# Optimization experiments

Measured on AMD Instinct MI355X. Metric: run time of the kernel, lower is better.

The kernel has to match this reference:

```python
import jax, jax.numpy as jnp
import numpy as np

B, T, HID, H = 2, 2048, 2048, 16
D = HID // H  # 128


def apply_rope(x):
    # Faithful port of the torch helper: treats x dims as (B, T, H, D)
    # regardless of the caller's actual layout (this reproduces the
    # original module's quirk of rotating q along the head axis).
    b, t, h, d = x.shape
    half = d // 2
    x1, x2 = x[..., :half], x[..., half:]
    theta = 1.0 / (10000.0 ** (jnp.arange(0, half, 2, dtype=jnp.float32) / half))
    pos = jnp.arange(t, dtype=jnp.float32)
    freq = pos[:, None] * theta[None, :]            # (t, half//2)
    sin = jnp.sin(freq)[None, :, None, :]
    cos = jnp.cos(freq)[None, :, None, :]
    x1e, x1o = x1[..., ::2], x1[..., 1::2]
    x2e, x2o = x2[..., ::2], x2[..., 1::2]
    x1r = jnp.concatenate([x1e * cos - x1o * sin, x1e * sin + x1o * cos], axis=-1)
    x2r = jnp.concatenate([x2e * cos - x2o * sin, x2e * sin + x2o * cos], axis=-1)
    return jnp.concatenate([x1r, x2r], axis=-1)


def setup_inputs() -> dict:
    key = jax.random.key(0)
    ks = jax.random.split(key, 5)
    s = 0.02
    return {
        "hidden_states": jax.random.normal(ks[0], (B, T, HID), dtype=jnp.float32),
        "Wq": jax.random.normal(ks[1], (HID, HID), dtype=jnp.float32) * s,
        "Wk": jax.random.normal(ks[2], (D, HID), dtype=jnp.float32) * s,
        "Wv": jax.random.normal(ks[3], (D, HID), dtype=jnp.float32) * s,
        "Wo": jax.random.normal(ks[4], (HID, HID), dtype=jnp.float32) * s,
    }


def reference(hidden_states, Wq, Wk, Wv, Wo):
    b, t, _ = hidden_states.shape
    scaling = D ** -0.5
    # projections (nn.Linear: x @ W.T)
    q = (hidden_states @ Wq.T).reshape(b, t, H, D).transpose(0, 2, 1, 3)  # (B,H,T,D)
    k = hidden_states @ Wk.T                                             # (B,T,D)
    v = hidden_states @ Wv.T                                             # (B,T,D)
    # RoPE applied exactly as in the torch module (note layout quirk)
    q = apply_rope(q)                 # rotated along head axis, as original
    k = apply_rope(k[:, None])        # (B,1,T,D): pos=0 -> permutation only
    v = v[:, None]                    # (B,1,T,D)
    scores = jnp.einsum("bhqd,bokd->bhqk", q, k) * scaling  # (B,H,T,T)
    causal = jnp.tril(jnp.ones((t, t), dtype=bool))
    scores = jnp.where(causal[None, None], scores, -jnp.inf)
    probs = jax.nn.softmax(scores, axis=-1)
    attn = jnp.einsum("bhqk,bokd->bhqd", probs, v)           # (B,H,T,D)
    attn = attn.transpose(0, 2, 1, 3).reshape(b, t, HID)
    return attn @ Wo.T
```

## Files before the change

kernel.cpp:

```cpp
#include <hip/hip_runtime.h>
#include <math.h>


typedef unsigned short u16;
typedef __attribute__((ext_vector_type(8))) short s16x8;
typedef __attribute__((ext_vector_type(4))) float f32x4;

#define B_   2
#define T_   2048
#define HID_ 2048
#define H_   16
#define D_   128

__device__ __forceinline__ u16 f2bf(float f) {
  unsigned u = __float_as_uint(f);
  unsigned r = ((u >> 16) & 1u) + 0x7fffu;
  return (u16)((u + r) >> 16);
}
__device__ __forceinline__ float bf2f(u16 b) {
  return __uint_as_float(((unsigned)b) << 16);
}

__global__ void cast_f32_to_bf16(const float* __restrict__ in,
                                 u16* __restrict__ out, int n4) {
  int i = blockIdx.x * blockDim.x + threadIdx.x;
  if (i >= n4) return;
  float4 v = reinterpret_cast<const float4*>(in)[i];
  ushort4 o;
  o.x = f2bf(v.x); o.y = f2bf(v.y); o.z = f2bf(v.z); o.w = f2bf(v.w);
  reinterpret_cast<ushort4*>(out)[i] = o;
}

__device__ __forceinline__ void gload_lds16(const u16* g, u16* lds) {
  __builtin_amdgcn_global_load_lds(
      (const __attribute__((address_space(1))) void*)g,
      (__attribute__((address_space(3))) void*)lds, 16, 0, 0);
}

template <int OUT_BF16>
__global__ __launch_bounds__(256) void gemm_bt(
    const u16* __restrict__ A, const u16* __restrict__ Bm,
    void* __restrict__ Cv, int M, int N, int K) {
  __shared__ __align__(16) u16 As[128 * 64];
  __shared__ __align__(16) u16 Bs[128 * 64];
  const int tid = threadIdx.x;
  const int w = tid >> 6, l = tid & 63;
  const int bm = blockIdx.x, bn = blockIdx.y;
  const int wm = (w >> 1) * 64, wn = (w & 1) * 64;
  const int lg = l >> 4, lc = l & 15;
  const int srow = l >> 3, slot = l & 7;
  f32x4 acc[4][4] = {};

  for (int k0 = 0; k0 < K; k0 += 64) {
#pragma unroll
    for (int i = 0; i < 4; ++i) {
      int R = (w * 4 + i) * 8;
      int row = R + srow;
      int c = slot ^ (row & 7);
      gload_lds16(A + (size_t)(bm * 128 + row) * K + k0 + c * 8, &As[R * 64]);
      gload_lds16(Bm + (size_t)(bn * 128 + row) * K + k0 + c * 8, &Bs[R * 64]);
    }
    __syncthreads();
#pragma unroll
    for (int kc = 0; kc < 2; ++kc) {
      s16x8 af[4], bfv[4];
#pragma unroll
      for (int mi = 0; mi < 4; ++mi) {
        int r = wm + mi * 16 + lc;
        int cc = kc * 4 + lg;
        af[mi] = *(const s16x8*)((const char*)As + r * 128 + ((cc ^ (r & 7)) * 16));
      }
#pragma unroll
      for (int ni = 0; ni < 4; ++ni) {
        int r = wn + ni * 16 + lc;
        int cc = kc * 4 + lg;
        bfv[ni] = *(const s16x8*)((const char*)Bs + r * 128 + ((cc ^ (r & 7)) * 16));
      }
#pragma unroll
      for (int mi = 0; mi < 4; ++mi)
#pragma unroll
        for (int ni = 0; ni < 4; ++ni)
          acc[mi][ni] = __builtin_amdgcn_mfma_f32_16x16x32_bf16(
              af[mi], bfv[ni], acc[mi][ni], 0, 0, 0);
    }
    __syncthreads();
  }
#pragma unroll
  for (int mi = 0; mi < 4; ++mi)
#pragma unroll
    for (int ni = 0; ni < 4; ++ni) {
      int mrow = bm * 128 + wm + mi * 16 + lg * 4;
      int ncol = bn * 128 + wn + ni * 16 + lc;
#pragma unroll
      for (int r = 0; r < 4; ++r) {
        float v = acc[mi][ni][r];
        if (OUT_BF16)
          ((u16*)Cv)[(size_t)(mrow + r) * N + ncol] = f2bf(v);
        else
          ((float*)Cv)[(size_t)(mrow + r) * N + ncol] = v;
      }
    }
}

__global__ void rope_q(u16* __restrict__ Q) {
  int idx = blockIdx.x * blockDim.x + threadIdx.x;
  int row = idx >> 10;
  int p = idx & 1023;
  int h = p >> 6;
  int i = p & 63;
  int j = i & 31;
  int d = (i < 32) ? (2 * i) : (64 + 2 * (i - 32));
  float theta = exp2f(-(float)j * (13.287712379549449f / 32.0f));
  float ang = (float)h * theta;
  float s, c;
  __sincosf(ang, &s, &c);
  unsigned* pq = (unsigned*)(Q + (size_t)row * HID_ + h * D_ + d);
  unsigned v = *pq;
  float a = bf2f((u16)(v & 0xffffu));
  float b = bf2f((u16)(v >> 16));
  *pq = ((unsigned)f2bf(a * s + b * c) << 16) | (unsigned)f2bf(a * c - b * s);
}

__global__ void transpose_v(const u16* __restrict__ V, u16* __restrict__ Vt) {
  int idx = blockIdx.x * blockDim.x + threadIdx.x;
  int t = idx & (T_ - 1);
  int d = (idx >> 11) & (D_ - 1);
  int b = idx >> 18;
  Vt[idx] = V[(size_t)(b * T_ + t) * D_ + d];
}

__global__ __launch_bounds__(256, 2) void mqa_attn(
    const u16* __restrict__ Q, const u16* __restrict__ K,
    const u16* __restrict__ Vt, u16* __restrict__ O) {
  __shared__ __align__(16) u16 Plds[4][2][16][72];
  const int tid = threadIdx.x;
  const int w = tid >> 6, l = tid & 63;
  const int lg = l >> 4, lc = l & 15;
  const int idx = blockIdx.x * 4 + w;
  const int h = blockIdx.y, b = blockIdx.z;
  const int ga = idx, gb = 127 - idx;
  const int q0a = ga * 16, q0b = gb * 16;
  const int nka = ga / 4 + 1, nkb = gb / 4 + 1;
  const u16* Kp = K + (size_t)b * T_ * D_;
  const u16* Vb = Vt + (size_t)b * D_ * T_;

  s16x8 qfa[4], qfb[4];
  {
    const u16* qa = Q + (size_t)(b * T_ + q0a + lc) * HID_ + h * D_ + lg * 8;
    const u16* qb = Q + (size_t)(b * T_ + q0b + lc) * HID_ + h * D_ + lg * 8;
#pragma unroll
    for (int kc = 0; kc < 4; ++kc) {
      qfa[kc] = *(const s16x8*)(qa + kc * 32);
      qfb[kc] = *(const s16x8*)(qb + kc * 32);
    }
  }

  float lA[4] = {0.f, 0.f, 0.f, 0.f}, lB[4] = {0.f, 0.f, 0.f, 0.f};
  f32x4 accA[8] = {}, accB[8] = {};
  const float scale = 0.08838834764831845f;

  for (int kt = 0; kt < nkb; ++kt) {
    const int kb = kt * 64;
    const bool doA = (kt < nka);
    f32x4 sacA[4], sacB[4];
    __builtin_amdgcn_s_setprio(1);
    if (doA) {
#pragma unroll
      for (int s = 0; s < 4; ++s) {
        const u16* kp = Kp + (size_t)(kb + s * 16 + lc) * D_ + lg * 8;
        s16x8 kf0 = *(const s16x8*)(kp);
        s16x8 kf1 = *(const s16x8*)(kp + 32);
        s16x8 kf2 = *(const s16x8*)(kp + 64);
        s16x8 kf3 = *(const s16x8*)(kp + 96);
        f32x4 aB = {0.f, 0.f, 0.f, 0.f};
        aB = __builtin_amdgcn_mfma_f32_16x16x32_bf16(qfb[0], kf0, aB, 0, 0, 0);
        aB = __builtin_amdgcn_mfma_f32_16x16x32_bf16(qfb[1], kf1, aB, 0, 0, 0);
        aB = __builtin_amdgcn_mfma_f32_16x16x32_bf16(qfb[2], kf2, aB, 0, 0, 0);
        aB = __builtin_amdgcn_mfma_f32_16x16x32_bf16(qfb[3], kf3, aB, 0, 0, 0);
        sacB[s] = aB;
        f32x4 aA = {0.f, 0.f, 0.f, 0.f};
        aA = __builtin_amdgcn_mfma_f32_16x16x32_bf16(qfa[0], kf0, aA, 0, 0, 0);
        aA = __builtin_amdgcn_mfma_f32_16x16x32_bf16(qfa[1], kf1, aA, 0, 0, 0);
        aA = __builtin_amdgcn_mfma_f32_16x16x32_bf16(qfa[2], kf2, aA, 0, 0, 0);
        aA = __builtin_amdgcn_mfma_f32_16x16x32_bf16(qfa[3], kf3, aA, 0, 0, 0);
        sacA[s] = aA;
      }
    } else {
#pragma unroll
      for (int s = 0; s < 4; ++s) {
        const u16* kp = Kp + (size_t)(kb + s * 16 + lc) * D_ + lg * 8;
        s16x8 kf0 = *(const s16x8*)(kp);
        s16x8 kf1 = *(const s16x8*)(kp + 32);
        s16x8 kf2 = *(const s16x8*)(kp + 64);
        s16x8 kf3 = *(const s16x8*)(kp + 96);
        f32x4 aB = {0.f, 0.f, 0.f, 0.f};
        aB = __builtin_amdgcn_mfma_f32_16x16x32_bf16(qfb[0], kf0, aB, 0, 0, 0);
        aB = __builtin_amdgcn_mfma_f32_16x16x32_bf16(qfb[1], kf1, aB, 0, 0, 0);
        aB = __builtin_amdgcn_mfma_f32_16x16x32_bf16(qfb[2], kf2, aB, 0, 0, 0);
        aB = __builtin_amdgcn_mfma_f32_16x16x32_bf16(qfb[3], kf3, aB, 0, 0, 0);
        sacB[s] = aB;
      }
    }
    __builtin_amdgcn_s_setprio(0);
    s16x8 vf0[8];
#pragma unroll
    for (int dt = 0; dt < 8; ++dt)
      vf0[dt] = *(const s16x8*)(Vb + (size_t)(dt * 16 + lc) * T_ + kb + lg * 8);
    {
      const bool lastc = (kt == nkb - 1);
#pragma unroll
      for (int r = 0; r < 4; ++r) {
        const int qabs = q0b + lg * 4 + r;
        float al = 0.f;
#pragma unroll
        for (int s = 0; s < 4; ++s) {
          float x = fminf(sacB[s][r] * scale, 30.f);
          if (lastc && (kb + s * 16 + lc > qabs)) x = -INFINITY;
          float pp = __expf(x);
          al += pp;
          Plds[w][1][lg * 4 + r][s * 16 + lc] = f2bf(pp);
        }
        lB[r] += al;
      }
    }
    if (doA) {
      const bool lastc = (kt == nka - 1);
#pragma unroll
      for (int r = 0; r < 4; ++r) {
        const int qabs = q0a + lg * 4 + r;
        float al = 0.f;
#pragma unroll
        for (int s = 0; s < 4; ++s) {
          float x = fminf(sacA[s][r] * scale, 30.f);
          if (lastc && (kb + s * 16 + lc > qabs)) x = -INFINITY;
          float pp = __expf(x);
          al += pp;
          Plds[w][0][lg * 4 + r][s * 16 + lc] = f2bf(pp);
        }
        lA[r] += al;
      }
    }
    {
      s16x8 paB = *(const s16x8*)&Plds[w][1][lc][lg * 8];
      __builtin_amdgcn_s_setprio(1);
      if (doA) {
        s16x8 paA = *(const s16x8*)&Plds[w][0][lc][lg * 8];
#pragma unroll
        for (int dt = 0; dt < 8; ++dt) {
          accB[dt] = __builtin_amdgcn_mfma_f32_16x16x32_bf16(paB, vf0[dt], accB[dt], 0, 0, 0);
          accA[dt] = __builtin_amdgcn_mfma_f32_16x16x32_bf16(paA, vf0[dt], accA[dt], 0, 0, 0);
        }
      } else {
#pragma unroll
        for (int dt = 0; dt < 8; ++dt)
          accB[dt] = __builtin_amdgcn_mfma_f32_16x16x32_bf16(paB, vf0[dt], accB[dt], 0, 0, 0);
      }
      __builtin_amdgcn_s_setprio(0);
    }
    {
      s16x8 paB = *(const s16x8*)&Plds[w][1][lc][32 + lg * 8];
      __builtin_amdgcn_s_setprio(1);
      if (doA) {
        s16x8 paA = *(const s16x8*)&Plds[w][0][lc][32 + lg * 8];
#pragma unroll
        for (int dt = 0; dt < 8; ++dt) {
          s16x8 vf = *(const s16x8*)(Vb + (size_t)(dt * 16 + lc) * T_ + kb + 32 + lg * 8);
          accB[dt] = __builtin_amdgcn_mfma_f32_16x16x32_bf16(paB, vf, accB[dt], 0, 0, 0);
          accA[dt] = __builtin_amdgcn_mfma_f32_16x16x32_bf16(paA, vf, accA[dt], 0, 0, 0);
        }
      } else {
#pragma unroll
        for (int dt = 0; dt < 8; ++dt) {
          s16x8 vf = *(const s16x8*)(Vb + (size_t)(dt * 16 + lc) * T_ + kb + 32 + lg * 8);
          accB[dt] = __builtin_amdgcn_mfma_f32_16x16x32_bf16(paB, vf, accB[dt], 0, 0, 0);
        }
      }
      __builtin_amdgcn_s_setprio(0);
    }
  }
#pragma unroll
  for (int m = 1; m < 16; m <<= 1)
#pragma unroll
    for (int r = 0; r < 4; ++r) {
      lA[r] += __shfl_xor(lA[r], m, 64);
      lB[r] += __shfl_xor(lB[r], m, 64);
    }
  u16* oa = O + (size_t)(b * T_ + q0a + lg * 4) * HID_ + h * D_ + lc;
  u16* ob = O + (size_t)(b * T_ + q0b + lg * 4) * HID_ + h * D_ + lc;
#pragma unroll
  for (int dt = 0; dt < 8; ++dt)
#pragma unroll
    for (int r = 0; r < 4; ++r) {
      oa[(size_t)r * HID_ + dt * 16] = f2bf(accA[dt][r] / lA[r]);
      ob[(size_t)r * HID_ + dt * 16] = f2bf(accB[dt][r] / lB[r]);
    }
}

extern "C" void kernel_launch(void* const* d_in, const int* in_sizes, int n_in,
                              void* d_out, int out_size, void* d_ws, size_t ws_size,
                              hipStream_t stream) {
  const float* hs = (const float*)d_in[0];
  const float* Wq = (const float*)d_in[1];
  const float* Wk = (const float*)d_in[2];
  const float* Wv = (const float*)d_in[3];
  const float* Wo = (const float*)d_in[4];
  float* out = (float*)d_out;
  char* ws = (char*)d_ws;

  u16* hb  = (u16*)(ws + 0);
  u16* wqb = (u16*)(ws + 16777216);
  u16* wkb = (u16*)(ws + 25165824);
  u16* wvb = (u16*)(ws + 25690112);
  u16* wob = (u16*)(ws + 26214400);
  u16* Qb  = (u16*)(ws + 34603008);
  u16* Kb  = (u16*)(ws + 51380224);
  u16* Vb  = (u16*)(ws + 52428800);
  u16* Vtb = (u16*)(ws + 53477376);
  u16* Ab  = (u16*)(ws + 54525952);

  cast_f32_to_bf16<<<8192, 256, 0, stream>>>(hs, hb, 2097152);
  cast_f32_to_bf16<<<4096, 256, 0, stream>>>(Wq, wqb, 1048576);
  cast_f32_to_bf16<<<256, 256, 0, stream>>>(Wk, wkb, 65536);
  cast_f32_to_bf16<<<256, 256, 0, stream>>>(Wv, wvb, 65536);
  cast_f32_to_bf16<<<4096, 256, 0, stream>>>(Wo, wob, 1048576);

  gemm_bt<1><<<dim3(32, 16), 256, 0, stream>>>(hb, wqb, Qb, 4096, 2048, 2048);
  gemm_bt<1><<<dim3(32, 1), 256, 0, stream>>>(hb, wkb, Kb, 4096, 128, 2048);
  gemm_bt<1><<<dim3(32, 1), 256, 0, stream>>>(hb, wvb, Vb, 4096, 128, 2048);

  rope_q<<<16384, 256, 0, stream>>>(Qb);
  transpose_v<<<2048, 256, 0, stream>>>(Vb, Vtb);

  mqa_attn<<<dim3(16, 16, 2), 256, 0, stream>>>(Qb, Kb, Vtb, Ab);

  gemm_bt<0><<<dim3(32, 16), 256, 0, stream>>>(Ab, wob, out, 4096, 2048, 2048);

  (void)in_sizes; (void)n_in; (void)out_size; (void)ws_size;
}
```

Before: 422.6 us.

## Widen attention key tile to 128 and interleave QK^T with softmax per subtile

Doubles the key block per loop iteration from 64 to 128 columns, which halves the number of loop trips and spreads the fixed per-iteration overhead over more work. The score computation is restructured so each 16-key subtile's MFMA result is exponentiated and written to LDS right away instead of being held for the whole block. This cuts live accumulator registers and lets the exp work overlap with the matrix ops. V prefetch now happens before the QK loop. The trade-off is more wasted masked work on the diagonal tile, which is now twice as wide, and a larger LDS buffer for P.

```diff
diff --git a/kernel.cpp b/kernel.cpp
--- a/kernel.cpp
+++ b/kernel.cpp
@@ -132,7 +132,7 @@
 __global__ __launch_bounds__(256, 2) void mqa_attn(
     const u16* __restrict__ Q, const u16* __restrict__ K,
     const u16* __restrict__ Vt, u16* __restrict__ O) {
-  __shared__ __align__(16) u16 Plds[4][2][16][72];
+  __shared__ __align__(16) u16 Plds[4][2][16][136];
   const int tid = threadIdx.x;
   const int w = tid >> 6, l = tid & 63;
   const int lg = l >> 4, lc = l & 15;
@@ -140,7 +140,7 @@
   const int h = blockIdx.y, b = blockIdx.z;
   const int ga = idx, gb = 127 - idx;
   const int q0a = ga * 16, q0b = gb * 16;
-  const int nka = ga / 4 + 1, nkb = gb / 4 + 1;
+  const int nka = ga / 8 + 1, nkb = gb / 8 + 1;
   const u16* Kp = K + (size_t)b * T_ * D_;
   const u16* Vb = Vt + (size_t)b * D_ * T_;
 
@@ -160,118 +160,73 @@
   const float scale = 0.08838834764831845f;
 
   for (int kt = 0; kt < nkb; ++kt) {
-    const int kb = kt * 64;
+    const int kb = kt * 128;
     const bool doA = (kt < nka);
-    f32x4 sacA[4], sacB[4];
-    __builtin_amdgcn_s_setprio(1);
-    if (doA) {
-#pragma unroll
-      for (int s = 0; s < 4; ++s) {
-        const u16* kp = Kp + (size_t)(kb + s * 16 + lc) * D_ + lg * 8;
-        s16x8 kf0 = *(const s16x8*)(kp);
-        s16x8 kf1 = *(const s16x8*)(kp + 32);
-        s16x8 kf2 = *(const s16x8*)(kp + 64);
-        s16x8 kf3 = *(const s16x8*)(kp + 96);
-        f32x4 aB = {0.f, 0.f, 0.f, 0.f};
-        aB = __builtin_amdgcn_mfma_f32_16x16x32_bf16(qfb[0], kf0, aB, 0, 0, 0);
-        aB = __builtin_amdgcn_mfma_f32_16x16x32_bf16(qfb[1], kf1, aB, 0, 0, 0);
-        aB = __builtin_amdgcn_mfma_f32_16x16x32_bf16(qfb[2], kf2, aB, 0, 0, 0);
-        aB = __builtin_amdgcn_mfma_f32_16x16x32_bf16(qfb[3], kf3, aB, 0, 0, 0);
-        sacB[s] = aB;
+    const bool lastA = (kt == nka - 1);
+    const bool lastB = (kt == nkb - 1);
+    s16x8 vf0[8];
+#pragma unroll
+    for (int dt = 0; dt < 8; ++dt)
+      vf0[dt] = *(const s16x8*)(Vb + (size_t)(dt * 16 + lc) * T_ + kb + lg * 8);
+#pragma unroll
+    for (int s = 0; s < 8; ++s) {
+      const u16* kp = Kp + (size_t)(kb + s * 16 + lc) * D_ + lg * 8;
+      s16x8 kf0 = *(const s16x8*)(kp);
+      s16x8 kf1 = *(const s16x8*)(kp + 32);
+      s16x8 kf2 = *(const s16x8*)(kp + 64);
+      s16x8 kf3 = *(const s16x8*)(kp + 96);
+      const int kcol = kb + s * 16 + lc;
+      __builtin_amdgcn_s_setprio(1);
+      f32x4 aB = {0.f, 0.f, 0.f, 0.f};
+      aB = __builtin_amdgcn_mfma_f32_16x16x32_bf16(qfb[0], kf0, aB, 0, 0, 0);
+      aB = __builtin_amdgcn_mfma_f32_16x16x32_bf16(qfb[1], kf1, aB, 0, 0, 0);
+      aB = __builtin_amdgcn_mfma_f32_16x16x32_bf16(qfb[2], kf2, aB, 0, 0, 0);
+      aB = __builtin_amdgcn_mfma_f32_16x16x32_bf16(qfb[3], kf3, aB, 0, 0, 0);
+      __builtin_amdgcn_s_setprio(0);
+#pragma unroll
+      for (int r = 0; r < 4; ++r) {
+        float x = fminf(aB[r] * scale, 30.f);
+        if (lastB && (kcol > q0b + lg * 4 + r)) x = -INFINITY;
+        float pp = __expf(x);
+        lB[r] += pp;
+        Plds[w][1][lg * 4 + r][s * 16 + lc] = f2bf(pp);
+      }
+      if (doA) {
+        __builtin_amdgcn_s_setprio(1);
         f32x4 aA = {0.f, 0.f, 0.f, 0.f};
         aA = __builtin_amdgcn_mfma_f32_16x16x32_bf16(qfa[0], kf0, aA, 0, 0, 0);
         aA = __builtin_amdgcn_mfma_f32_16x16x32_bf16(qfa[1], kf1, aA, 0, 0, 0);
         aA = __builtin_amdgcn_mfma_f32_16x16x32_bf16(qfa[2], kf2, aA, 0, 0, 0);
         aA = __builtin_amdgcn_mfma_f32_16x16x32_bf16(qfa[3], kf3, aA, 0, 0, 0);
-        sacA[s] = aA;
-      }
-    } else {
-#pragma unroll
-      for (int s = 0; s < 4; ++s) {
-        const u16* kp = Kp + (size_t)(kb + s * 16 + lc) * D_ + lg * 8;
-        s16x8 kf0 = *(const s16x8*)(kp);
-        s16x8 kf1 = *(const s16x8*)(kp + 32);
-        s16x8 kf2 = *(const s16x8*)(kp + 64);
-        s16x8 kf3 = *(const s16x8*)(kp + 96);
-        f32x4 aB = {0.f, 0.f, 0.f, 0.f};
-        aB = __builtin_amdgcn_mfma_f32_16x16x32_bf16(qfb[0], kf0, aB, 0, 0, 0);
-        aB = __builtin_amdgcn_mfma_f32_16x16x32_bf16(qfb[1], kf1, aB, 0, 0, 0);
-        aB = __builtin_amdgcn_mfma_f32_16x16x32_bf16(qfb[2], kf2, aB, 0, 0, 0);
-        aB = __builtin_amdgcn_mfma_f32_16x16x32_bf16(qfb[3], kf3, aB, 0, 0, 0);
-        sacB[s] = aB;
-      }
-    }
-    __builtin_amdgcn_s_setprio(0);
-    s16x8 vf0[8];
-#pragma unroll
-    for (int dt = 0; dt < 8; ++dt)
-      vf0[dt] = *(const s16x8*)(Vb + (size_t)(dt * 16 + lc) * T_ + kb + lg * 8);
-    {
-      const bool lastc = (kt == nkb - 1);
-#pragma unroll
-      for (int r = 0; r < 4; ++r) {
-        const int qabs = q0b + lg * 4 + r;
-        float al = 0.f;
-#pragma unroll
-        for (int s = 0; s < 4; ++s) {
-          float x = fminf(sacB[s][r] * scale, 30.f);
-          if (lastc && (kb + s * 16 + lc > qabs)) x = -INFINITY;
+        __builtin_amdgcn_s_setprio(0);
+#pragma unroll
+        for (int r = 0; r < 4; ++r) {
+          float x = fminf(aA[r] * scale, 30.f);
+          if (lastA && (kcol > q0a + lg * 4 + r)) x = -INFINITY;
           float pp = __expf(x);
-          al += pp;
-          Plds[w][1][lg * 4 + r][s * 16 + lc] = f2bf(pp);
-        }
-        lB[r] += al;
-      }
-    }
-    if (doA) {
-      const bool lastc = (kt == nka - 1);
-#pragma unroll
-      for (int r = 0; r < 4; ++r) {
-        const int qabs = q0a + lg * 4 + r;
-        float al = 0.f;
-#pragma unroll
-        for (int s = 0; s < 4; ++s) {
-          float x = fminf(sacA[s][r] * scale, 30.f);
-          if (lastc && (kb + s * 16 + lc > qabs)) x = -INFINITY;
-          float pp = __expf(x);
-          al += pp;
+          lA[r] += pp;
           Plds[w][0][lg * 4 + r][s * 16 + lc] = f2bf(pp);
         }
-        lA[r] += al;
-      }
-    }
-    {
-      s16x8 paB = *(const s16x8*)&Plds[w][1][lc][lg * 8];
+      }
+    }
+#pragma unroll
+    for (int ph = 0; ph < 4; ++ph) {
+      s16x8 paB = *(const s16x8*)&Plds[w][1][lc][ph * 32 + lg * 8];
       __builtin_amdgcn_s_setprio(1);
       if (doA) {
-        s16x8 paA = *(const s16x8*)&Plds[w][0][lc][lg * 8];
+        s16x8 paA = *(const s16x8*)&Plds[w][0][lc][ph * 32 + lg * 8];
 #pragma unroll
         for (int dt = 0; dt < 8; ++dt) {
-          accB[dt] = __builtin_amdgcn_mfma_f32_16x16x32_bf16(paB, vf0[dt], accB[dt], 0, 0, 0);
-          accA[dt] = __builtin_amdgcn_mfma_f32_16x16x32_bf16(paA, vf0[dt], accA[dt], 0, 0, 0);
-        }
-      } else {
-#pragma unroll
-        for (int dt = 0; dt < 8; ++dt)
-          accB[dt] = __builtin_amdgcn_mfma_f32_16x16x32_bf16(paB, vf0[dt], accB[dt], 0, 0, 0);
-      }
-      __builtin_amdgcn_s_setprio(0);
-    }
-    {
-      s16x8 paB = *(const s16x8*)&Plds[w][1][lc][32 + lg * 8];
-      __builtin_amdgcn_s_setprio(1);
-      if (doA) {
-        s16x8 paA = *(const s16x8*)&Plds[w][0][lc][32 + lg * 8];
-#pragma unroll
-        for (int dt = 0; dt < 8; ++dt) {
-          s16x8 vf = *(const s16x8*)(Vb + (size_t)(dt * 16 + lc) * T_ + kb + 32 + lg * 8);
+          s16x8 vf = (ph == 0) ? vf0[dt]
+                   : *(const s16x8*)(Vb + (size_t)(dt * 16 + lc) * T_ + kb + ph * 32 + lg * 8);
           accB[dt] = __builtin_amdgcn_mfma_f32_16x16x32_bf16(paB, vf, accB[dt], 0, 0, 0);
           accA[dt] = __builtin_amdgcn_mfma_f32_16x16x32_bf16(paA, vf, accA[dt], 0, 0, 0);
         }
       } else {
 #pragma unroll
         for (int dt = 0; dt < 8; ++dt) {
-          s16x8 vf = *(const s16x8*)(Vb + (size_t)(dt * 16 + lc) * T_ + kb + 32 + lg * 8);
+          s16x8 vf = (ph == 0) ? vf0[dt]
+                   : *(const s16x8*)(Vb + (size_t)(dt * 16 + lc) * T_ + kb + ph * 32 + lg * 8);
           accB[dt] = __builtin_amdgcn_mfma_f32_16x16x32_bf16(paB, vf, accB[dt], 0, 0, 0);
         }
       }
```

After: 428.9 us. Within noise of the previous version (+1.5%).
